# Performance work log

Measured on AMD Instinct MI355X. Metric: run time of the kernel, lower is better.

## Reference

```python
import jax, jax.numpy as jnp
import numpy as np

N = 100000   # nodes
E = 1600000  # edges
B = 256      # graphs
EPS = 1e-5   # batchnorm eps


def setup_inputs() -> dict:
    key = jax.random.key(0)
    ks = jax.random.split(key, 20)
    inp = {
        "x": jax.random.normal(ks[0], (N, 22), dtype=jnp.float32),
        "edge_index": jax.random.randint(ks[1], (2, E), 0, N, dtype=jnp.int64),
        "batch": jnp.sort(jax.random.randint(ks[2], (N,), 0, B, dtype=jnp.int64)),
        # GCNConv weights (x @ W + b convention)
        "W1": jax.random.normal(ks[3], (22, 64), dtype=jnp.float32) * 0.2,
        "b1": jnp.zeros((64,), dtype=jnp.float32),
        "W2": jax.random.normal(ks[4], (64, 64), dtype=jnp.float32) * 0.12,
        "b2": jnp.zeros((64,), dtype=jnp.float32),
        "W3": jax.random.normal(ks[5], (64, 128), dtype=jnp.float32) * 0.12,
        "b3": jnp.zeros((128,), dtype=jnp.float32),
        # BatchNorm1d params + running stats (eval mode)
        "g1": jax.random.uniform(ks[6], (64,), minval=0.5, maxval=1.5),
        "be1": jax.random.normal(ks[7], (64,)) * 0.1,
        "m1": jax.random.normal(ks[8], (64,)) * 0.1,
        "v1": jax.random.uniform(ks[9], (64,), minval=0.5, maxval=1.5),
        "g2": jax.random.uniform(ks[10], (64,), minval=0.5, maxval=1.5),
        "be2": jax.random.normal(ks[11], (64,)) * 0.1,
        "m2": jax.random.normal(ks[12], (64,)) * 0.1,
        "v2": jax.random.uniform(ks[13], (64,), minval=0.5, maxval=1.5),
    }
    return inp


def _gcn_conv(h, W, b, src, dst, norm_e, dinv):
    # PyG GCNConv: h' = D^{-1/2}(A+I)D^{-1/2} (h W) + b
    h = h @ W                                             # [N, F]
    msg = h[src] * norm_e[:, None]                        # gather + scale [E, F]
    agg = jax.ops.segment_sum(msg, dst, num_segments=N)   # scatter-add
    agg = agg + h * dinv[:, None]                         # self-loop term
    return agg + b


def _bn_eval(x, g, be, m, v):
    return (x - m) * jax.lax.rsqrt(v + EPS) * g + be


def reference(x, edge_index, batch, W1, b1, W2, b2, W3, b3,
              g1, be1, m1, v1, g2, be2, m2, v2):
    src, dst = edge_index[0], edge_index[1]
    # degree with self-loops (computed on target nodes, symmetric norm)
    deg = jax.ops.segment_sum(jnp.ones((E,), x.dtype), dst, num_segments=N) + 1.0
    dis = jax.lax.rsqrt(deg)            # deg^{-1/2}, deg >= 1
    norm_e = dis[src] * dis[dst]        # per-edge norm
    dinv = dis * dis                    # 1/deg for self-loop edges

    h = jax.nn.relu(_bn_eval(_gcn_conv(x, W1, b1, src, dst, norm_e, dinv), g1, be1, m1, v1))
    h = jax.nn.relu(_bn_eval(_gcn_conv(h, W2, b2, src, dst, norm_e, dinv), g2, be2, m2, v2))
    h = jax.nn.relu(_gcn_conv(h, W3, b3, src, dst, norm_e, dinv))

    # global mean pool over graph ids
    sums = jax.ops.segment_sum(h, batch, num_segments=B)              # [B, 128]
    cnts = jax.ops.segment_sum(jnp.ones((N,), h.dtype), batch, num_segments=B)
    return sums / jnp.maximum(cnts, 1.0)[:, None]
```

## Files before the change

### kernel.cpp

```cpp
#include <hip/hip_runtime.h>

#define BN_EPS 1e-5f

typedef _Float16 half_t;
typedef _Float16 half4 __attribute__((ext_vector_type(4)));
typedef _Float16 half8 __attribute__((ext_vector_type(8)));
typedef unsigned int u32;
typedef unsigned short u16;

__device__ __forceinline__ float norm_of(u32 w) {
    u16 hb = (u16)(w & 0x7fffu);
    return (float)__builtin_bit_cast(half_t, hb);
}


#define EPB 4096

__global__ void k_bhist(const int* __restrict__ dst, int* __restrict__ countsT,
                        int nblk, int e) {
    __shared__ int h[256];
    h[threadIdx.x] = 0;
    __syncthreads();
    int base = blockIdx.x * EPB;
    int end = min(base + EPB, e);
    for (int i = base + threadIdx.x; i < end; i += 256)
        atomicAdd(&h[dst[i] >> 9], 1);
    __syncthreads();
    countsT[threadIdx.x * nblk + blockIdx.x] = h[threadIdx.x];
}

__global__ void k_colscan(int* __restrict__ countsT, int* __restrict__ colSum, int nblk) {
    __shared__ int lds[256];
    int t = threadIdx.x;
    int* col = countsT + (size_t)blockIdx.x * nblk;
    int carry = 0;
    for (int base = 0; base < nblk; base += 512) {
        int i0 = base + t * 2, i1 = i0 + 1;
        int v0 = (i0 < nblk) ? col[i0] : 0;
        int v1 = (i1 < nblk) ? col[i1] : 0;
        int s = v0 + v1;
        int val = s;
        lds[t] = val;
        __syncthreads();
        for (int off = 1; off < 256; off <<= 1) {
            int tmp = (t >= off) ? lds[t - off] : 0;
            __syncthreads();
            val += tmp;
            lds[t] = val;
            __syncthreads();
        }
        int run = carry + val - s;
        if (i0 < nblk) col[i0] = run;
        if (i1 < nblk) col[i1] = run + v0;
        carry += lds[255];
        __syncthreads();
    }
    if (t == 0) colSum[blockIdx.x] = carry;
}

__global__ void k_bbase(const int* __restrict__ colSum, int* __restrict__ bucketBase) {
    __shared__ int lds[256];
    int t = threadIdx.x;
    int s = colSum[t];
    int val = s;
    lds[t] = val;
    __syncthreads();
    for (int off = 1; off < 256; off <<= 1) {
        int tmp = (t >= off) ? lds[t - off] : 0;
        __syncthreads();
        val += tmp;
        lds[t] = val;
        __syncthreads();
    }
    bucketBase[t] = val - s;
    if (t == 255) bucketBase[256] = val;
}

__global__ void k_bscatter(const int* __restrict__ src, const int* __restrict__ dst,
                           const int* __restrict__ countsT, const int* __restrict__ bucketBase,
                           u32* __restrict__ rec, int nblk, int e) {
    __shared__ int cur[256];
    cur[threadIdx.x] = countsT[threadIdx.x * nblk + blockIdx.x] + bucketBase[threadIdx.x];
    __syncthreads();
    int base = blockIdx.x * EPB;
    int end = min(base + EPB, e);
    for (int i = base + threadIdx.x; i < end; i += 256) {
        int d = dst[i], s = src[i];
        int pos = atomicAdd(&cur[d >> 9], 1);
        rec[pos] = ((u32)s << 9) | (u32)(d & 511);
    }
}

__global__ void k_bmake1(const u32* __restrict__ rec, const int* __restrict__ bucketBase,
                         int* __restrict__ rowptr, float* __restrict__ dis,
                         float* __restrict__ dinv, int n) {
    __shared__ int h[512];
    __shared__ int ps[256];
    int t = threadIdx.x;
    h[t] = 0; h[t + 256] = 0;
    __syncthreads();
    int beg = bucketBase[blockIdx.x];
    int end = bucketBase[blockIdx.x + 1];
    for (int i = beg + t; i < end; i += 256)
        atomicAdd(&h[rec[i] & 511], 1);
    __syncthreads();
    int node0 = blockIdx.x << 9;
    int d0 = h[2 * t], d1 = h[2 * t + 1];
    int pair = d0 + d1;
    ps[t] = pair;
    __syncthreads();
    int val = pair;
    for (int off = 1; off < 256; off <<= 1) {
        int tmp = (t >= off) ? ps[t - off] : 0;
        __syncthreads();
        val += tmp;
        ps[t] = val;
        __syncthreads();
    }
    int excl0 = beg + val - pair;
    int nodeA = node0 + 2 * t, nodeB = nodeA + 1;
    if (nodeA <= n) rowptr[nodeA] = excl0;
    if (nodeB <= n) rowptr[nodeB] = excl0 + d0;
    if (nodeA < n) { float dd = (float)(d0 + 1); dis[nodeA] = rsqrtf(dd); dinv[nodeA] = 1.0f / dd; }
    if (nodeB < n) { float dd = (float)(d1 + 1); dis[nodeB] = rsqrtf(dd); dinv[nodeB] = 1.0f / dd; }
    if ((n & 511) == 0 && blockIdx.x == gridDim.x - 1 && t == 255) rowptr[n] = end;
}

__global__ void k_bfill(const u32* __restrict__ rec, const int* __restrict__ bucketBase,
                        const int* __restrict__ rowptr, const float* __restrict__ dis,
                        u32* __restrict__ csr, int n) {
    __shared__ int cur[512];
    __shared__ float disl[512];
    int t = threadIdx.x;
    int node0 = blockIdx.x << 9;
    for (int j = t; j < 512; j += 256) {
        int node = node0 + j;
        cur[j]  = (node < n) ? rowptr[node] : 0;
        disl[j] = (node < n) ? dis[node] : 0.0f;
    }
    __syncthreads();
    int beg = bucketBase[blockIdx.x];
    int end = bucketBase[blockIdx.x + 1];
    for (int i = beg + t; i < end; i += 256) {
        u32 r = rec[i];
        int dl = r & 511;
        int s = (int)(r >> 9);
        int pos = atomicAdd(&cur[dl], 1);
        half_t hh = (half_t)(dis[s] * disl[dl]);
        csr[pos] = ((u32)s << 15) | (u32)__builtin_bit_cast(u16, hh);
    }
}


__global__ void k_x2h(const float* __restrict__ X, half_t* __restrict__ Xh, int n) {
    int i = blockIdx.x * blockDim.x + threadIdx.x;
    if (i >= n * 24) return;
    int node = i / 24, c = i % 24;
    Xh[i] = (c < 22) ? (half_t)X[(size_t)node * 22 + c] : (half_t)0.0f;
}


__global__ void k_gather22h(const half_t* __restrict__ Xh, const int* __restrict__ rowptr,
                            const u32* __restrict__ csr, const float* __restrict__ dinv,
                            half_t* __restrict__ out, int n) {
    int node = blockIdx.x * 4 + (threadIdx.x >> 6);
    if (node >= n) return;
    int lane = threadIdx.x & 63;
    int esub = lane >> 3;
    int sub  = lane & 7;
    bool act = sub < 6;
    const half4* X4 = (const half4*)Xh;
    int beg = rowptr[node], end = rowptr[node + 1];
    float4 a0 = make_float4(0, 0, 0, 0), a1 = a0;
    for (int e = beg; e < end; e += 16) {
        int i0 = e + esub, i1 = e + 8 + esub;
        u32 w0 = csr[min(i0, end - 1)];
        u32 w1 = csr[min(i1, end - 1)];
        if (act && i0 < end) {
            float nn = norm_of(w0);
            half4 h = X4[(size_t)(w0 >> 15) * 6 + sub];
            a0.x = fmaf((float)h.x, nn, a0.x); a0.y = fmaf((float)h.y, nn, a0.y);
            a0.z = fmaf((float)h.z, nn, a0.z); a0.w = fmaf((float)h.w, nn, a0.w);
        }
        if (act && i1 < end) {
            float nn = norm_of(w1);
            half4 h = X4[(size_t)(w1 >> 15) * 6 + sub];
            a1.x = fmaf((float)h.x, nn, a1.x); a1.y = fmaf((float)h.y, nn, a1.y);
            a1.z = fmaf((float)h.z, nn, a1.z); a1.w = fmaf((float)h.w, nn, a1.w);
        }
    }
    float4 a;
    a.x = a0.x + a1.x; a.y = a0.y + a1.y; a.z = a0.z + a1.z; a.w = a0.w + a1.w;
#pragma unroll
    for (int d = 8; d <= 32; d <<= 1) {
        a.x += __shfl_xor(a.x, d); a.y += __shfl_xor(a.y, d);
        a.z += __shfl_xor(a.z, d); a.w += __shfl_xor(a.w, d);
    }
    if (esub == 0 && act) {
        float di = dinv[node];
        half4 hs = X4[(size_t)node * 6 + sub];
        half4 r;
        r.x = (half_t)fmaf((float)hs.x, di, a.x);
        r.y = (half_t)fmaf((float)hs.y, di, a.y);
        r.z = (half_t)fmaf((float)hs.z, di, a.z);
        r.w = (half_t)fmaf((float)hs.w, di, a.w);
        ((half4*)out)[(size_t)node * 6 + sub] = r;
    }
}

__global__ void k_gather64h(const half_t* __restrict__ H, const int* __restrict__ rowptr,
                            const u32* __restrict__ csr, const float* __restrict__ dinv,
                            half_t* __restrict__ out, int n) {
    int node = blockIdx.x * 4 + (threadIdx.x >> 6);
    if (node >= n) return;
    int lane = threadIdx.x & 63;
    int esub = lane >> 3;
    int sub  = lane & 7;
    const half8* H8 = (const half8*)H;
    int beg = rowptr[node], end = rowptr[node + 1];
    float a0[8], a1[8];
#pragma unroll
    for (int j = 0; j < 8; ++j) { a0[j] = 0.0f; a1[j] = 0.0f; }
    for (int e = beg; e < end; e += 16) {
        int i0 = e + esub, i1 = e + 8 + esub;
        u32 w0 = csr[min(i0, end - 1)];
        u32 w1 = csr[min(i1, end - 1)];
        if (i0 < end) {
            float nn = norm_of(w0);
            half8 h = H8[(size_t)(w0 >> 15) * 8 + sub];
#pragma unroll
            for (int j = 0; j < 8; ++j) a0[j] = fmaf((float)h[j], nn, a0[j]);
        }
        if (i1 < end) {
            float nn = norm_of(w1);
            half8 h = H8[(size_t)(w1 >> 15) * 8 + sub];
#pragma unroll
            for (int j = 0; j < 8; ++j) a1[j] = fmaf((float)h[j], nn, a1[j]);
        }
    }
    float acc[8];
#pragma unroll
    for (int j = 0; j < 8; ++j) acc[j] = a0[j] + a1[j];
#pragma unroll
    for (int d = 8; d <= 32; d <<= 1) {
#pragma unroll
        for (int j = 0; j < 8; ++j) acc[j] += __shfl_xor(acc[j], d);
    }
    if (esub == 0) {
        float di = dinv[node];
        half8 hs = H8[(size_t)node * 8 + sub];
        half8 r;
#pragma unroll
        for (int j = 0; j < 8; ++j) r[j] = (half_t)fmaf((float)hs[j], di, acc[j]);
        ((half8*)out)[(size_t)node * 8 + sub] = r;
    }
}


__global__ void k_prep_all(const float* __restrict__ W1, const float* __restrict__ b1,
                           const float* __restrict__ g1, const float* __restrict__ be1,
                           const float* __restrict__ m1, const float* __restrict__ v1,
                           const float* __restrict__ W2, const float* __restrict__ b2,
                           const float* __restrict__ g2, const float* __restrict__ be2,
                           const float* __restrict__ m2, const float* __restrict__ v2,
                           const float* __restrict__ W3, const float* __restrict__ b3,
                           float* __restrict__ Wp1, float* __restrict__ C1,
                           float* __restrict__ Wp2, float* __restrict__ C2,
                           float* __restrict__ Wp3, float* __restrict__ C3) {
    int i = blockIdx.x * blockDim.x + threadIdx.x;
    if (i < 24 * 64) {
        int r = i / 64, c = i % 64;
        float A = g1[c] * rsqrtf(v1[c] + BN_EPS);
        Wp1[i] = (r < 22) ? W1[r * 64 + c] * A : 0.0f;
        if (i < 64) C1[i] = be1[i] + (b1[i] - m1[i]) * A;
    }
    int j = i - 24 * 64;
    if (j >= 0 && j < 64 * 64) {
        int c = j % 64;
        float A = g2[c] * rsqrtf(v2[c] + BN_EPS);
        Wp2[j] = W2[j] * A;
        if (j < 64) C2[j] = be2[j] + (b2[j] - m2[j]) * A;
    }
    int k = i - 24 * 64 - 64 * 64;
    if (k >= 0 && k < 64 * 128) {
        Wp3[k] = W3[k];
        if (k < 128) C3[k] = b3[k];
    }
}


template <int FIN, int FOUT>
__global__ __launch_bounds__(256) void k_gemm2(const half_t* __restrict__ P,
                                               const float* __restrict__ Wp,
                                               const float* __restrict__ Cf,
                                               half_t* __restrict__ outp, int n) {
    constexpr int COLS = FOUT / 4;
    int lane = threadIdx.x & 63;
    int part = __builtin_amdgcn_readfirstlane(threadIdx.x >> 6);
    int node = blockIdx.x * 64 + lane;
    if (node >= n) return;

    half8 xr[FIN / 8];
    const half8* p8 = (const half8*)(P + (size_t)node * FIN);
#pragma unroll
    for (int i = 0; i < FIN / 8; ++i) xr[i] = p8[i];
    const half_t* x = (const half_t*)xr;

    const float* wq = Wp + part * COLS;
    const float* cq = Cf + part * COLS;

#pragma unroll 1
    for (int c0 = 0; c0 < COLS; c0 += 16) {
        float4 a0 = make_float4(0, 0, 0, 0), a1 = a0, a2 = a0, a3 = a0;
        const float* wbase = wq + c0;
#pragma unroll
        for (int k = 0; k < FIN; ++k) {
            float xv = (float)x[k];
            const float4* wr = (const float4*)(wbase + k * FOUT);
            float4 w0 = wr[0], w1 = wr[1], w2 = wr[2], w3 = wr[3];
            a0.x = fmaf(xv, w0.x, a0.x); a0.y = fmaf(xv, w0.y, a0.y);
            a0.z = fmaf(xv, w0.z, a0.z); a0.w = fmaf(xv, w0.w, a0.w);
            a1.x = fmaf(xv, w1.x, a1.x); a1.y = fmaf(xv, w1.y, a1.y);
            a1.z = fmaf(xv, w1.z, a1.z); a1.w = fmaf(xv, w1.w, a1.w);
            a2.x = fmaf(xv, w2.x, a2.x); a2.y = fmaf(xv, w2.y, a2.y);
            a2.z = fmaf(xv, w2.z, a2.z); a2.w = fmaf(xv, w2.w, a2.w);
            a3.x = fmaf(xv, w3.x, a3.x); a3.y = fmaf(xv, w3.y, a3.y);
            a3.z = fmaf(xv, w3.z, a3.z); a3.w = fmaf(xv, w3.w, a3.w);
        }
        const float4* c4 = (const float4*)(cq + c0);
        float4 cA = c4[0], cB = c4[1], cC = c4[2], cD = c4[3];
        half8 h0, h1;
        h0[0] = (half_t)fmaxf(a0.x + cA.x, 0.0f); h0[1] = (half_t)fmaxf(a0.y + cA.y, 0.0f);
        h0[2] = (half_t)fmaxf(a0.z + cA.z, 0.0f); h0[3] = (half_t)fmaxf(a0.w + cA.w, 0.0f);
        h0[4] = (half_t)fmaxf(a1.x + cB.x, 0.0f); h0[5] = (half_t)fmaxf(a1.y + cB.y, 0.0f);
        h0[6] = (half_t)fmaxf(a1.z + cB.z, 0.0f); h0[7] = (half_t)fmaxf(a1.w + cB.w, 0.0f);
        h1[0] = (half_t)fmaxf(a2.x + cC.x, 0.0f); h1[1] = (half_t)fmaxf(a2.y + cC.y, 0.0f);
        h1[2] = (half_t)fmaxf(a2.z + cC.z, 0.0f); h1[3] = (half_t)fmaxf(a2.w + cC.w, 0.0f);
        h1[4] = (half_t)fmaxf(a3.x + cD.x, 0.0f); h1[5] = (half_t)fmaxf(a3.y + cD.y, 0.0f);
        h1[6] = (half_t)fmaxf(a3.z + cD.z, 0.0f); h1[7] = (half_t)fmaxf(a3.w + cD.w, 0.0f);
        half8* oh = (half8*)(outp + (size_t)node * FOUT + part * COLS + c0);
        oh[0] = h0;
        oh[1] = h1;
    }
}


__global__ __launch_bounds__(256) void k_gemm3pool(const half_t* __restrict__ P,
                                                   const float* __restrict__ Wp,
                                                   const float* __restrict__ Cf,
                                                   const int* __restrict__ batch,
                                                   float* __restrict__ sums, int n) {
    constexpr int FIN = 64, FOUT = 128, COLS = 32;
    __shared__ half_t tile[128][66];
    __shared__ int batl[64];
    int lane = threadIdx.x & 63;
    int part = __builtin_amdgcn_readfirstlane(threadIdx.x >> 6);
    int node = blockIdx.x * 64 + lane;
    bool valid = node < n;

    if (threadIdx.x < 64) {
        int nd = blockIdx.x * 64 + threadIdx.x;
        batl[threadIdx.x] = (nd < n) ? batch[nd] : -1;
    }

    half8 xr[FIN / 8];
    if (valid) {
        const half8* p8 = (const half8*)(P + (size_t)node * FIN);
#pragma unroll
        for (int i = 0; i < FIN / 8; ++i) xr[i] = p8[i];
    } else {
#pragma unroll
        for (int i = 0; i < FIN / 8; ++i) xr[i] = half8{};
    }
    const half_t* x = (const half_t*)xr;
    const float* wq = Wp + part * COLS;
    const float* cq = Cf + part * COLS;

#pragma unroll 1
    for (int c0 = 0; c0 < COLS; c0 += 16) {
        float4 a0 = make_float4(0, 0, 0, 0), a1 = a0, a2 = a0, a3 = a0;
        const float* wbase = wq + c0;
#pragma unroll
        for (int k = 0; k < FIN; ++k) {
            float xv = (float)x[k];
            const float4* wr = (const float4*)(wbase + k * FOUT);
            float4 w0 = wr[0], w1 = wr[1], w2 = wr[2], w3 = wr[3];
            a0.x = fmaf(xv, w0.x, a0.x); a0.y = fmaf(xv, w0.y, a0.y);
            a0.z = fmaf(xv, w0.z, a0.z); a0.w = fmaf(xv, w0.w, a0.w);
            a1.x = fmaf(xv, w1.x, a1.x); a1.y = fmaf(xv, w1.y, a1.y);
            a1.z = fmaf(xv, w1.z, a1.z); a1.w = fmaf(xv, w1.w, a1.w);
            a2.x = fmaf(xv, w2.x, a2.x); a2.y = fmaf(xv, w2.y, a2.y);
            a2.z = fmaf(xv, w2.z, a2.z); a2.w = fmaf(xv, w2.w, a2.w);
            a3.x = fmaf(xv, w3.x, a3.x); a3.y = fmaf(xv, w3.y, a3.y);
            a3.z = fmaf(xv, w3.z, a3.z); a3.w = fmaf(xv, w3.w, a3.w);
        }
        const float4* c4 = (const float4*)(cq + c0);
        float4 cA = c4[0], cB = c4[1], cC = c4[2], cD = c4[3];
        int r0 = part * COLS + c0;
        tile[r0 +  0][lane] = (half_t)fmaxf(a0.x + cA.x, 0.0f);
        tile[r0 +  1][lane] = (half_t)fmaxf(a0.y + cA.y, 0.0f);
        tile[r0 +  2][lane] = (half_t)fmaxf(a0.z + cA.z, 0.0f);
        tile[r0 +  3][lane] = (half_t)fmaxf(a0.w + cA.w, 0.0f);
        tile[r0 +  4][lane] = (half_t)fmaxf(a1.x + cB.x, 0.0f);
        tile[r0 +  5][lane] = (half_t)fmaxf(a1.y + cB.y, 0.0f);
        tile[r0 +  6][lane] = (half_t)fmaxf(a1.z + cB.z, 0.0f);
        tile[r0 +  7][lane] = (half_t)fmaxf(a1.w + cB.w, 0.0f);
        tile[r0 +  8][lane] = (half_t)fmaxf(a2.x + cC.x, 0.0f);
        tile[r0 +  9][lane] = (half_t)fmaxf(a2.y + cC.y, 0.0f);
        tile[r0 + 10][lane] = (half_t)fmaxf(a2.z + cC.z, 0.0f);
        tile[r0 + 11][lane] = (half_t)fmaxf(a2.w + cC.w, 0.0f);
        tile[r0 + 12][lane] = (half_t)fmaxf(a3.x + cD.x, 0.0f);
        tile[r0 + 13][lane] = (half_t)fmaxf(a3.y + cD.y, 0.0f);
        tile[r0 + 14][lane] = (half_t)fmaxf(a3.z + cD.z, 0.0f);
        tile[r0 + 15][lane] = (half_t)fmaxf(a3.w + cD.w, 0.0f);
    }
    __syncthreads();
    if (threadIdx.x < 128) {
        int col = threadIdx.x;
        int cur = batl[0];
        float acc = 0.0f;
        for (int i = 0; i < 64; ++i) {
            int b = batl[i];
            if (b < 0) break;
            if (b != cur) { atomicAdd(&sums[cur * 128 + col], acc); acc = 0.0f; cur = b; }
            acc += (float)tile[col][i];
        }
        if (cur >= 0) atomicAdd(&sums[cur * 128 + col], acc);
    }
}

__global__ void k_pool_div(const float* __restrict__ sums, const int* __restrict__ batch,
                           float* __restrict__ out, int n, int nB) {
    int i = blockIdx.x * blockDim.x + threadIdx.x;
    if (i >= nB * 128) return;
    int b = i >> 7;
    int lo = 0, hi = n;
    while (lo < hi) { int mid = (lo + hi) >> 1; if (batch[mid] < b) lo = mid + 1; else hi = mid; }
    int start = lo;
    lo = 0; hi = n;
    while (lo < hi) { int mid = (lo + hi) >> 1; if (batch[mid] < b + 1) lo = mid + 1; else hi = mid; }
    float cnt = (float)(lo - start);
    out[i] = sums[i] / fmaxf(cnt, 1.0f);
}


extern "C" void kernel_launch(void* const* d_in, const int* in_sizes, int n_in,
                              void* d_out, int out_size, void* d_ws, size_t ws_size,
                              hipStream_t stream) {
    const float* x   = (const float*)d_in[0];
    const int*   ei  = (const int*)d_in[1];
    const int*   bat = (const int*)d_in[2];
    const float* W1  = (const float*)d_in[3];
    const float* b1  = (const float*)d_in[4];
    const float* W2  = (const float*)d_in[5];
    const float* b2  = (const float*)d_in[6];
    const float* W3  = (const float*)d_in[7];
    const float* b3  = (const float*)d_in[8];
    const float* g1  = (const float*)d_in[9];
    const float* be1 = (const float*)d_in[10];
    const float* m1  = (const float*)d_in[11];
    const float* v1  = (const float*)d_in[12];
    const float* g2  = (const float*)d_in[13];
    const float* be2 = (const float*)d_in[14];
    const float* m2  = (const float*)d_in[15];
    const float* v2  = (const float*)d_in[16];

    const int N = in_sizes[0] / 22;
    const int E = in_sizes[1] / 2;
    const int B = out_size / 128;
    const int* src = ei;
    const int* dst = ei + E;

    const int nblk = (E + EPB - 1) / EPB;
    const int NBKT = (N + 511) >> 9;

    size_t off = 0;
    char* base = (char*)d_ws;
    auto alloc = [&](size_t bytes) -> void* {
        void* p = base + off;
        off = (off + bytes + 255) & ~(size_t)255;
        return p;
    };
    int*    rowptr = (int*)alloc((size_t)(N + 1) * 4);
    int*    countsT = (int*)alloc((size_t)nblk * 256 * 4);
    int*    colSum = (int*)alloc(256 * 4);
    int*    bucketBase = (int*)alloc(257 * 4);
    u32*    rec    = (u32*)alloc((size_t)E * 4);
    float*  dis    = (float*)alloc((size_t)N * 4);
    float*  dinv   = (float*)alloc((size_t)N * 4);
    u32*    csr    = (u32*)alloc((size_t)E * 4);
    half_t* Xh     = (half_t*)alloc((size_t)N * 24 * 2);
    half_t* Hh1    = (half_t*)alloc((size_t)N * 64 * 2);
    half_t* Hh2    = (half_t*)alloc((size_t)N * 64 * 2);
    half_t* aggH   = (half_t*)alloc((size_t)N * 64 * 2);
    float*  sums   = (float*)alloc((size_t)B * 128 * 4);
    float*  Wp1    = (float*)alloc(24 * 64 * 4);
    float*  Wp2    = (float*)alloc(64 * 64 * 4);
    float*  Wp3    = (float*)alloc(64 * 128 * 4);
    float*  C1     = (float*)alloc(64 * 4);
    float*  C2     = (float*)alloc(64 * 4);
    float*  C3     = (float*)alloc(128 * 4);

    const int T = 256;
    auto blk = [](long long n, int t) { return (int)((n + t - 1) / t); };

    k_prep_all<<<blk(24 * 64 + 64 * 64 + 64 * 128, T), T, 0, stream>>>(
        W1, b1, g1, be1, m1, v1, W2, b2, g2, be2, m2, v2, W3, b3,
        Wp1, C1, Wp2, C2, Wp3, C3);

    k_bhist<<<nblk, T, 0, stream>>>(dst, countsT, nblk, E);
    k_colscan<<<256, T, 0, stream>>>(countsT, colSum, nblk);
    k_bbase<<<1, 256, 0, stream>>>(colSum, bucketBase);
    k_bscatter<<<nblk, T, 0, stream>>>(src, dst, countsT, bucketBase, rec, nblk, E);
    k_bmake1<<<NBKT, T, 0, stream>>>(rec, bucketBase, rowptr, dis, dinv, N);
    k_bfill<<<NBKT, T, 0, stream>>>(rec, bucketBase, rowptr, dis, csr, N);

    k_x2h<<<blk((long long)N * 24, T), T, 0, stream>>>(x, Xh, N);

    k_gather22h<<<blk(N, 4), T, 0, stream>>>(Xh, rowptr, csr, dinv, aggH, N);
    k_gemm2<24, 64><<<blk(N, 64), T, 0, stream>>>(aggH, Wp1, C1, Hh1, N);

    k_gather64h<<<blk(N, 4), T, 0, stream>>>(Hh1, rowptr, csr, dinv, aggH, N);
    k_gemm2<64, 64><<<blk(N, 64), T, 0, stream>>>(aggH, Wp2, C2, Hh2, N);

    k_gather64h<<<blk(N, 4), T, 0, stream>>>(Hh2, rowptr, csr, dinv, aggH, N);
    hipMemsetAsync(sums, 0, (size_t)B * 128 * sizeof(float), stream);
    k_gemm3pool<<<blk(N, 64), T, 0, stream>>>(aggH, Wp3, C3, bat, sums, N);

    k_pool_div<<<blk(B * 128, T), T, 0, stream>>>(sums, bat, (float*)d_out, N, B);
}
```

Measured before the change: 352.0 us.

## Pack two nodes per wavefront in 64-wide gather; fold bucket-base scan into scatter

The 64-feature gather kernel now gives each node half a wavefront (32 lanes, 4 edge slots) instead of a full wavefront with 8 edge slots. Average degree is about 16, so this is meant to cut idle lanes and shorten the shuffle reduction. The bucket scatter kernel now recomputes the 256-entry bucket-base prefix scan itself from colSum, so it no longer waits on the separate k_bbase launch, which now runs after it for the later kernels. The cost is a redundant scan in every scatter block, plus an unused helper function left in the code.

```diff
diff --git a/kernel.cpp b/kernel.cpp
--- a/kernel.cpp
+++ b/kernel.cpp
@@ -58,6 +58,53 @@
     if (t == 0) colSum[blockIdx.x] = carry;
 }
 
+__device__ __forceinline__ int bucket_base_of(const int* colSum, int* lds, int want) {
+    int t = threadIdx.x;
+    int s = colSum[t];
+    int val = s;
+    lds[t] = val;
+    __syncthreads();
+    for (int off = 1; off < 256; off <<= 1) {
+        int tmp = (t >= off) ? lds[t - off] : 0;
+        __syncthreads();
+        val += tmp;
+        lds[t] = val;
+        __syncthreads();
+    }
+    int r = (want == 0) ? 0 : lds[want - 1];
+    __syncthreads();
+    return r;
+}
+
+__global__ void k_bscatter(const int* __restrict__ src, const int* __restrict__ dst,
+                           const int* __restrict__ countsT, const int* __restrict__ colSum,
+                           u32* __restrict__ rec, int nblk, int e) {
+    __shared__ int lds[256];
+    __shared__ int cur[256];
+    int t = threadIdx.x;
+    int s = colSum[t];
+    int val = s;
+    lds[t] = val;
+    __syncthreads();
+    for (int off = 1; off < 256; off <<= 1) {
+        int tmp = (t >= off) ? lds[t - off] : 0;
+        __syncthreads();
+        val += tmp;
+        lds[t] = val;
+        __syncthreads();
+    }
+    int basev = val - s;
+    cur[t] = countsT[t * nblk + blockIdx.x] + basev;
+    __syncthreads();
+    int base = blockIdx.x * EPB;
+    int end = min(base + EPB, e);
+    for (int i = base + t; i < end; i += 256) {
+        int d = dst[i], sv = src[i];
+        int pos = atomicAdd(&cur[d >> 9], 1);
+        rec[pos] = ((u32)sv << 9) | (u32)(d & 511);
+    }
+}
+
 __global__ void k_bbase(const int* __restrict__ colSum, int* __restrict__ bucketBase) {
     __shared__ int lds[256];
     int t = threadIdx.x;
@@ -74,21 +121,6 @@
     }
     bucketBase[t] = val - s;
     if (t == 255) bucketBase[256] = val;
-}
-
-__global__ void k_bscatter(const int* __restrict__ src, const int* __restrict__ dst,
-                           const int* __restrict__ countsT, const int* __restrict__ bucketBase,
-                           u32* __restrict__ rec, int nblk, int e) {
-    __shared__ int cur[256];
-    cur[threadIdx.x] = countsT[threadIdx.x * nblk + blockIdx.x] + bucketBase[threadIdx.x];
-    __syncthreads();
-    int base = blockIdx.x * EPB;
-    int end = min(base + EPB, e);
-    for (int i = base + threadIdx.x; i < end; i += 256) {
-        int d = dst[i], s = src[i];
-        int pos = atomicAdd(&cur[d >> 9], 1);
-        rec[pos] = ((u32)s << 9) | (u32)(d & 511);
-    }
 }
 
 __global__ void k_bmake1(const u32* __restrict__ rec, const int* __restrict__ bucketBase,
@@ -211,18 +243,20 @@
 __global__ void k_gather64h(const half_t* __restrict__ H, const int* __restrict__ rowptr,
                             const u32* __restrict__ csr, const float* __restrict__ dinv,
                             half_t* __restrict__ out, int n) {
-    int node = blockIdx.x * 4 + (threadIdx.x >> 6);
+    int lane = threadIdx.x & 63;
+    int nsub = lane >> 5;
+    int hl   = lane & 31;
+    int esub = hl >> 3;
+    int sub  = hl & 7;
+    int node = blockIdx.x * 8 + (int)(threadIdx.x >> 6) * 2 + nsub;
     if (node >= n) return;
-    int lane = threadIdx.x & 63;
-    int esub = lane >> 3;
-    int sub  = lane & 7;
     const half8* H8 = (const half8*)H;
     int beg = rowptr[node], end = rowptr[node + 1];
     float a0[8], a1[8];
 #pragma unroll
     for (int j = 0; j < 8; ++j) { a0[j] = 0.0f; a1[j] = 0.0f; }
-    for (int e = beg; e < end; e += 16) {
-        int i0 = e + esub, i1 = e + 8 + esub;
+    for (int e = beg; e < end; e += 8) {
+        int i0 = e + esub, i1 = e + 4 + esub;
         u32 w0 = csr[min(i0, end - 1)];
         u32 w1 = csr[min(i1, end - 1)];
         if (i0 < end) {
@@ -242,7 +276,7 @@
 #pragma unroll
     for (int j = 0; j < 8; ++j) acc[j] = a0[j] + a1[j];
 #pragma unroll
-    for (int d = 8; d <= 32; d <<= 1) {
+    for (int d = 8; d <= 16; d <<= 1) {
 #pragma unroll
         for (int j = 0; j < 8; ++j) acc[j] += __shfl_xor(acc[j], d);
     }
@@ -510,8 +544,8 @@
 
     k_bhist<<<nblk, T, 0, stream>>>(dst, countsT, nblk, E);
     k_colscan<<<256, T, 0, stream>>>(countsT, colSum, nblk);
+    k_bscatter<<<nblk, T, 0, stream>>>(src, dst, countsT, colSum, rec, nblk, E);
     k_bbase<<<1, 256, 0, stream>>>(colSum, bucketBase);
-    k_bscatter<<<nblk, T, 0, stream>>>(src, dst, countsT, bucketBase, rec, nblk, E);
     k_bmake1<<<NBKT, T, 0, stream>>>(rec, bucketBase, rowptr, dis, dinv, N);
     k_bfill<<<NBKT, T, 0, stream>>>(rec, bucketBase, rowptr, dis, csr, N);
 
@@ -520,10 +554,10 @@
     k_gather22h<<<blk(N, 4), T, 0, stream>>>(Xh, rowptr, csr, dinv, aggH, N);
     k_gemm2<24, 64><<<blk(N, 64), T, 0, stream>>>(aggH, Wp1, C1, Hh1, N);
 
-    k_gather64h<<<blk(N, 4), T, 0, stream>>>(Hh1, rowptr, csr, dinv, aggH, N);
+    k_gather64h<<<blk(N, 8), T, 0, stream>>>(Hh1, rowptr, csr, dinv, aggH, N);
     k_gemm2<64, 64><<<blk(N, 64), T, 0, stream>>>(aggH, Wp2, C2, Hh2, N);
 
-    k_gather64h<<<blk(N, 4), T, 0, stream>>>(Hh2, rowptr, csr, dinv, aggH, N);
+    k_gather64h<<<blk(N, 8), T, 0, stream>>>(Hh2, rowptr, csr, dinv, aggH, N);
     hipMemsetAsync(sums, 0, (size_t)B * 128 * sizeof(float), stream);
     k_gemm3pool<<<blk(N, 64), T, 0, stream>>>(aggH, Wp3, C3, bat, sums, N);
 
```

After: 336.6 us. -4.4%, faster.
